# Performance work log

Hardware: AMD Instinct MI355X
Metric: run time of the kernel (lower is better)

## Reference

```python
import jax, jax.numpy as jnp
import numpy as np
import math

DIM = 1024
NUM_HEADS = 16
HEAD_DIM = DIM // NUM_HEADS
ROPE_BASE = 10000.0
LN_EPS = 1e-5


def _rope_tables(seq_len):
    inv_freq = 1.0 / (ROPE_BASE ** (jnp.arange(0, HEAD_DIM, 2, dtype=jnp.float32) / HEAD_DIM))
    t = jnp.arange(seq_len, dtype=jnp.float32)
    freqs = t[:, None] * inv_freq[None, :]            # (T, D/2)
    emb = jnp.concatenate([freqs, freqs], axis=-1)    # (T, D)
    return jnp.cos(emb), jnp.sin(emb)


def _rotate_half(x):
    x1 = x[..., ::2]
    x2 = x[..., 1::2]
    return jnp.stack((-x2, x1), axis=-1).reshape(x.shape)


def _heads(y):
    B, T, _ = y.shape
    return y.reshape(B, T, NUM_HEADS, HEAD_DIM).transpose(0, 2, 1, 3)  # (B,H,T,hd)


def _layernorm(x, w, b):
    mu = jnp.mean(x, axis=-1, keepdims=True)
    var = jnp.var(x, axis=-1, keepdims=True)
    return (x - mu) / jnp.sqrt(var + LN_EPS) * w + b


def setup_inputs() -> dict:
    key = jax.random.key(0)
    ks = jax.random.split(key, 16)
    s = 1.0 / math.sqrt(DIM)
    d = {
        "x": jax.random.normal(ks[0], (2, 2048, DIM), jnp.float32),
        "h_a": jax.random.normal(ks[1], (2, 512, DIM), jnp.float32),
        "h_t": jax.random.normal(ks[2], (2, 64, DIM), jnp.float32),
        "p": jax.random.normal(ks[3], (2, 256, DIM), jnp.float32),
    }
    names = ["Wq", "Wks", "Wvs", "Wka", "Wva", "Wkt", "Wvt", "Wo", "Wf"]
    for i, n in enumerate(names):
        d[n] = jax.random.normal(ks[4 + i], (DIM, DIM), jnp.float32) * s
        d["b" + n[1:]] = jnp.zeros((DIM,), jnp.float32)
    d["gating"] = jnp.zeros((1,), jnp.float32)
    d["ln_w"] = jnp.ones((DIM,), jnp.float32)
    d["ln_b"] = jnp.zeros((DIM,), jnp.float32)
    return d


def reference(x, h_a, h_t, p,
              Wq, bq, Wks, bks, Wvs, bvs, Wka, bka, Wva, bva,
              Wkt, bkt, Wvt, bvt, Wo, bo, Wf, bf,
              gating, ln_w, ln_b):
    B, T, D = x.shape
    g = jnp.tanh(gating)[0]
    h_adapter = jnp.concatenate((h_a, p), axis=1)          # (B, Ta+Tp, D)
    cos, sin = _rope_tables(T)                             # (T, hd)

    q = _heads(x @ Wq + bq)
    ks_ = _heads(x @ Wks + bks)
    vs = _heads(x @ Wvs + bvs)
    q = q * cos + _rotate_half(q) * sin
    ks_ = ks_ * cos + _rotate_half(ks_) * sin

    ka = _heads(h_adapter @ Wka + bka)
    va = _heads(h_adapter @ Wva + bva)
    kt = _heads(h_t @ Wkt + bkt)
    vt = _heads(h_t @ Wvt + bvt)

    s_self = jnp.einsum("bhqd,bhkd->bhqk", q, ks_)
    s_adpt = jnp.einsum("bhqd,bhkd->bhqk", q, ka)
    s_task = jnp.einsum("bhqd,bhkd->bhqk", q, kt) * g
    scores = jnp.concatenate([s_self, s_adpt, s_task], axis=-1) / math.sqrt(HEAD_DIM)
    attn = jax.nn.softmax(scores, axis=-1)                 # (B,H,T,S_total)

    v_all = jnp.concatenate([vs, va, vt], axis=2)          # (B,H,S_total,hd)
    out = jnp.einsum("bhqk,bhkd->bhqd", attn, v_all)
    out = out.transpose(0, 2, 1, 3).reshape(B, T, D)
    out = out @ Wo + bo

    res = _layernorm(out + x, ln_w, ln_b)
    res = jax.nn.relu(res @ Wf + bf)
    return res
```

## Files before the change

kernel.cpp:

```cpp
#include <hip/hip_runtime.h>

typedef __attribute__((ext_vector_type(8))) short bf16x8;
typedef __attribute__((ext_vector_type(4))) float f32x4;
typedef __attribute__((ext_vector_type(8))) unsigned short u16x8;
typedef __attribute__((ext_vector_type(4))) unsigned short u16x4;

#define DEV static __device__ __forceinline__

DEV float bf2f(unsigned short u) {
    union { unsigned int i; float f; } x; x.i = ((unsigned int)u) << 16; return x.f;
}
DEV unsigned short f2bf(float f) {
    union { float f; unsigned int i; } x; x.f = f;
    unsigned int r = x.i + 0x7FFFu + ((x.i >> 16) & 1u);
    return (unsigned short)(r >> 16);
}
DEV unsigned int cvt_pk_bf16(float a, float b) {
    unsigned int r;
    asm("v_cvt_pk_bf16_f32 %0, %1, %2" : "=v"(r) : "v"(a), "v"(b));
    return r;
}
DEV float ldany(const void* p, size_t i, bool f32) {
    return f32 ? ((const float*)p)[i] : bf2f(((const unsigned short*)p)[i]);
}
DEV void gload16(const void* g, void* l) {
    __builtin_amdgcn_global_load_lds(
        (const __attribute__((address_space(1))) unsigned int*)g,
        reinterpret_cast<__attribute__((address_space(3))) unsigned int*>(
            reinterpret_cast<uintptr_t>(l)),
        16, 0, 0);
}

struct Quad { const void* w0; const void* w1; const void* w2; const void* w3; };
struct Tri  { const void* b0; const void* b1; const void* b2; void* o0; void* o1; void* o2; };
struct ExtArgs {
    const void* ha; const void* pp; const void* ht;
    const void* bka; const void* bva; const void* bkt; const void* bvt;
    void* kx; void* vx;
};

__global__ __launch_bounds__(256)
void rope_tab(float2* __restrict__ tab, const unsigned int* __restrict__ wchk,
              int* __restrict__ flag)
{
    const int idx = blockIdx.x * 256 + threadIdx.x;
    if (idx == 0) flag[0] = (wchk[0] == 0x3F800000u) ? 1 : 0;
    const int m = idx >> 5, d = idx & 31;
    const float a = (float)m * exp2f(-(float)d * 0.41524101186092033f);
    float sn, cs;
    sincosf(a, &sn, &cs);
    tab[idx] = make_float2(cs, sn);
}

__global__ __launch_bounds__(256)
void transpose_w(Quad q, unsigned short* __restrict__ dstbase, const int* __restrict__ flagp)
{
    const bool dsf = (*flagp != 0);
    const int z = blockIdx.z;
    const void* W = (z == 0) ? q.w0 : (z == 1) ? q.w1 : (z == 2) ? q.w2 : q.w3;
    unsigned short* out = dstbase + ((size_t)z << 20);
    __shared__ unsigned short Ts[64][72];
    const int t = threadIdx.x;
    const int n0 = blockIdx.x * 64, k0 = blockIdx.y * 64;
    const int r = t >> 2, c = (t & 3) << 4;
    if (!dsf) {
        const unsigned short* Wp = (const unsigned short*)W + (size_t)(k0 + r) * 1024 + n0 + c;
        *(u16x8*)&Ts[r][c]     = *(const u16x8*)Wp;
        *(u16x8*)&Ts[r][c + 8] = *(const u16x8*)(Wp + 8);
    } else {
        const float4* Wf4 = (const float4*)((const float*)W + (size_t)(k0 + r) * 1024 + n0 + c);
        float4 f[4];
        #pragma unroll
        for (int j = 0; j < 4; ++j) f[j] = Wf4[j];
        unsigned int* Td = (unsigned int*)&Ts[r][c];
        #pragma unroll
        for (int j = 0; j < 4; ++j) {
            Td[2 * j]     = cvt_pk_bf16(f[j].x, f[j].y);
            Td[2 * j + 1] = cvt_pk_bf16(f[j].z, f[j].w);
        }
    }
    __syncthreads();
    unsigned short tmp[16];
    #pragma unroll
    for (int j = 0; j < 16; ++j) tmp[j] = Ts[c + j][r];
    unsigned short* op = out + (size_t)(n0 + r) * 1024 + k0 + c;
    *(u16x8*)op       = *(const u16x8*)&tmp[0];
    *(u16x8*)(op + 8) = *(const u16x8*)&tmp[8];
}

template<int AMODE, int OMODE, bool RELU, bool ROPEF>
__global__ __launch_bounds__(256)
void gemm_mfma(const void* __restrict__ A, const unsigned short* __restrict__ WTbase,
               Tri t3, const int* __restrict__ flagp, const float2* __restrict__ rtab,
               int mblocks, int rpb_in, int rpb_out, int row_off)
{
    const int K = 1024, N = 1024;
    const bool dsf = (*flagp != 0);
    const bool af32 = (AMODE == 1) && dsf;
    __shared__ unsigned short As[2][64 * 64];
    __shared__ unsigned short Bs[2][128 * 64];
    const int tid = threadIdx.x;
    const int z = blockIdx.y / mblocks;
    const int m0 = (blockIdx.y - z * mblocks) * 64;
    const int n0 = blockIdx.x * 128;
    const unsigned short* WT = WTbase + ((size_t)z << 20);
    const void* bias = (z == 0) ? t3.b0 : (z == 1) ? t3.b1 : t3.b2;
    void* Cv = (z == 0) ? t3.o0 : (z == 1) ? t3.o1 : t3.o2;

    const int lane = tid & 63, wv = tid >> 6;
    const int l3 = lane >> 3, c8 = lane & 7;
    const int swz = (c8 ^ l3) << 3;

    const unsigned short* Bsrc[4];
    #pragma unroll
    for (int j = 0; j < 4; ++j)
        Bsrc[j] = WT + (size_t)(n0 + (wv << 5) + (j << 3) + l3) * K + swz;
    const unsigned short* Asrc[2];
    #pragma unroll
    for (int j = 0; j < 2; ++j)
        Asrc[j] = (const unsigned short*)A + (size_t)(m0 + (wv << 4) + (j << 3) + l3) * K + swz;

    const int ar = tid >> 2, aq = (tid & 3) << 1, ah = ar & 7;
    const size_t arow = (size_t)(m0 + ar) * K + (aq << 3);

    const int wm = (wv >> 1) << 5, wn = (wv & 1) << 6;
    const int il = lane & 15, quad = lane >> 4;
    const int h = il & 7;
    const int c0 = ((quad ^ h) << 3);
    int aoff[2], boff[4];
    #pragma unroll
    for (int mi = 0; mi < 2; ++mi) aoff[mi] = (wm + mi * 16 + il) * 64;
    #pragma unroll
    for (int nj = 0; nj < 4; ++nj) boff[nj] = (wn + nj * 16 + il) * 64;

    f32x4 acc[2][4];
    #pragma unroll
    for (int mi = 0; mi < 2; ++mi)
        #pragma unroll
        for (int nj = 0; nj < 4; ++nj) acc[mi][nj] = (f32x4){0.f, 0.f, 0.f, 0.f};

    u16x8 av[2];
    auto loadA = [&](int kq) {
        if (!af32) {
            const unsigned short* Ag = (const unsigned short*)A + arow + kq;
            av[0] = *(const u16x8*)Ag;
            av[1] = *(const u16x8*)(Ag + 8);
        } else {
            const float4* Af4 = (const float4*)((const float*)A + arow + kq);
            float4 f[4];
            #pragma unroll
            for (int j = 0; j < 4; ++j) f[j] = Af4[j];
            #pragma unroll
            for (int j = 0; j < 2; ++j) {
                unsigned int* d = (unsigned int*)&av[j];
                d[0] = cvt_pk_bf16(f[2 * j].x, f[2 * j].y);
                d[1] = cvt_pk_bf16(f[2 * j].z, f[2 * j].w);
                d[2] = cvt_pk_bf16(f[2 * j + 1].x, f[2 * j + 1].y);
                d[3] = cvt_pk_bf16(f[2 * j + 1].z, f[2 * j + 1].w);
            }
        }
    };
    auto writeA = [&](int buf) {
        *(u16x8*)&As[buf][ar * 64 + ((aq ^ ah) << 3)]       = av[0];
        *(u16x8*)&As[buf][ar * 64 + (((aq ^ 1) ^ ah) << 3)] = av[1];
    };
    auto stageB = [&](int buf, int k0) {
        #pragma unroll
        for (int j = 0; j < 4; ++j)
            gload16(Bsrc[j] + k0, &Bs[buf][((wv << 2) + j) << 9]);
    };
    auto stageA = [&](int buf, int k0) {
        #pragma unroll
        for (int j = 0; j < 2; ++j)
            gload16(Asrc[j] + k0, &As[buf][((wv << 1) + j) << 9]);
    };

    if (AMODE == 1) loadA(0);
    stageB(0, 0);
    if (AMODE == 1) { writeA(0); loadA(64); }
    else            stageA(0, 0);
    __syncthreads();

    for (int k0 = 0; k0 < K; k0 += 64) {
        const int cur = (k0 >> 6) & 1;
        if (k0 + 64 < K) {
            stageB(cur ^ 1, k0 + 64);
            if (AMODE == 1) { writeA(cur ^ 1); if (k0 + 128 < K) loadA(k0 + 128); }
            else            stageA(cur ^ 1, k0 + 64);
        }
        #pragma unroll
        for (int kk = 0; kk < 2; ++kk) {
            const int cc = c0 ^ (kk << 5);
            bf16x8 af[2], bfr[4];
            #pragma unroll
            for (int mi = 0; mi < 2; ++mi) af[mi] = *(const bf16x8*)&As[cur][aoff[mi] + cc];
            #pragma unroll
            for (int nj = 0; nj < 4; ++nj) bfr[nj] = *(const bf16x8*)&Bs[cur][boff[nj] + cc];
            #pragma unroll
            for (int mi = 0; mi < 2; ++mi)
                #pragma unroll
                for (int nj = 0; nj < 4; ++nj)
                    acc[mi][nj] = __builtin_amdgcn_mfma_f32_16x16x32_bf16(
                        af[mi], bfr[nj], acc[mi][nj], 0, 0, 0);
        }
        __syncthreads();
    }

    const bool doRope = ROPEF && (z < 2);
    float bval[4];
    #pragma unroll
    for (int nj = 0; nj < 4; ++nj) bval[nj] = ldany(bias, n0 + wn + nj * 16 + il, dsf);
    #pragma unroll
    for (int mi = 0; mi < 2; ++mi) {
        #pragma unroll
        for (int r = 0; r < 4; ++r) {
            const int m = m0 + wm + mi * 16 + quad * 4 + r;
            const int bidx = m / rpb_in;
            const size_t orow = (size_t)bidx * rpb_out + row_off + (m - bidx * rpb_in);
            #pragma unroll
            for (int nj = 0; nj < 4; ++nj) {
                float v = acc[mi][nj][r] + bval[nj];
                if (doRope) {
                    const int dcol = n0 + wn + nj * 16 + il;
                    const float2 cs2 = rtab[((m & 2047) << 5) | (dcol & 31)];
                    const float partner = __shfl_xor(v, 1);
                    v = (il & 1) ? fmaf(v, cs2.x, partner * cs2.y)
                                 : fmaf(v, cs2.x, -partner * cs2.y);
                }
                if (RELU) v = fmaxf(v, 0.0f);
                const size_t idx = orow * N + n0 + wn + nj * 16 + il;
                if (OMODE == 0) ((unsigned short*)Cv)[idx] = f2bf(v);
                else {
                    if (dsf) ((float*)Cv)[idx] = v;
                    else     ((unsigned short*)Cv)[idx] = f2bf(v);
                }
            }
        }
    }
}

__global__ __launch_bounds__(256)
void gemm_ext(ExtArgs ea, const unsigned short* __restrict__ WTbase,
              const int* __restrict__ flagp)
{
    const int K = 1024, N = 1024;
    const bool dsf = (*flagp != 0);
    __shared__ unsigned short As[2][64 * 64];
    __shared__ unsigned short Bs[2][128 * 64];
    const int tid = threadIdx.x;
    const int y = blockIdx.y;
    const int w = (y >= 26) ? 1 : 0;
    const int yy = y - w * 26;
    int s, m0b;
    if (yy < 16)      { s = 0; m0b = yy; }
    else if (yy < 24) { s = 1; m0b = yy - 16; }
    else              { s = 2; m0b = yy - 24; }
    const void* A = (s == 0) ? ea.ha : (s == 1) ? ea.pp : ea.ht;
    const int rpb_in  = (s == 0) ? 512 : (s == 1) ? 256 : 64;
    const int row_off = (s == 0) ? 0 : (s == 1) ? 512 : 768;
    const int wtslot = ((s == 2) ? 2 : 0) + w;
    const void* bias = (w == 0) ? ((s == 2) ? ea.bkt : ea.bka)
                                : ((s == 2) ? ea.bvt : ea.bva);
    void* Cv = (w == 0) ? ea.kx : ea.vx;
    const int m0 = m0b * 64;
    const int n0 = blockIdx.x * 128;
    const unsigned short* WT = WTbase + ((size_t)wtslot << 20);

    const int lane = tid & 63, wv = tid >> 6;
    const int l3 = lane >> 3, c8 = lane & 7;
    const int swz = (c8 ^ l3) << 3;

    const unsigned short* Bsrc[4];
    #pragma unroll
    for (int j = 0; j < 4; ++j)
        Bsrc[j] = WT + (size_t)(n0 + (wv << 5) + (j << 3) + l3) * K + swz;

    const int ar = tid >> 2, aq = (tid & 3) << 1, ah = ar & 7;
    const size_t arow = (size_t)(m0 + ar) * K + (aq << 3);

    const int wm = (wv >> 1) << 5, wn = (wv & 1) << 6;
    const int il = lane & 15, quad = lane >> 4;
    const int h = il & 7;
    const int c0 = ((quad ^ h) << 3);
    int aoff[2], boff[4];
    #pragma unroll
    for (int mi = 0; mi < 2; ++mi) aoff[mi] = (wm + mi * 16 + il) * 64;
    #pragma unroll
    for (int nj = 0; nj < 4; ++nj) boff[nj] = (wn + nj * 16 + il) * 64;

    f32x4 acc[2][4];
    #pragma unroll
    for (int mi = 0; mi < 2; ++mi)
        #pragma unroll
        for (int nj = 0; nj < 4; ++nj) acc[mi][nj] = (f32x4){0.f, 0.f, 0.f, 0.f};

    u16x8 av[2];
    auto loadA = [&](int kq) {
        if (!dsf) {
            const unsigned short* Ag = (const unsigned short*)A + arow + kq;
            av[0] = *(const u16x8*)Ag;
            av[1] = *(const u16x8*)(Ag + 8);
        } else {
            const float4* Af4 = (const float4*)((const float*)A + arow + kq);
            float4 f[4];
            #pragma unroll
            for (int j = 0; j < 4; ++j) f[j] = Af4[j];
            #pragma unroll
            for (int j = 0; j < 2; ++j) {
                unsigned int* d = (unsigned int*)&av[j];
                d[0] = cvt_pk_bf16(f[2 * j].x, f[2 * j].y);
                d[1] = cvt_pk_bf16(f[2 * j].z, f[2 * j].w);
                d[2] = cvt_pk_bf16(f[2 * j + 1].x, f[2 * j + 1].y);
                d[3] = cvt_pk_bf16(f[2 * j + 1].z, f[2 * j + 1].w);
            }
        }
    };
    auto writeA = [&](int buf) {
        *(u16x8*)&As[buf][ar * 64 + ((aq ^ ah) << 3)]       = av[0];
        *(u16x8*)&As[buf][ar * 64 + (((aq ^ 1) ^ ah) << 3)] = av[1];
    };
    auto stageB = [&](int buf, int k0) {
        #pragma unroll
        for (int j = 0; j < 4; ++j)
            gload16(Bsrc[j] + k0, &Bs[buf][((wv << 2) + j) << 9]);
    };

    loadA(0);
    stageB(0, 0);
    writeA(0); loadA(64);
    __syncthreads();

    for (int k0 = 0; k0 < K; k0 += 64) {
        const int cur = (k0 >> 6) & 1;
        if (k0 + 64 < K) {
            stageB(cur ^ 1, k0 + 64);
            writeA(cur ^ 1);
            if (k0 + 128 < K) loadA(k0 + 128);
        }
        #pragma unroll
        for (int kk = 0; kk < 2; ++kk) {
            const int cc = c0 ^ (kk << 5);
            bf16x8 af[2], bfr[4];
            #pragma unroll
            for (int mi = 0; mi < 2; ++mi) af[mi] = *(const bf16x8*)&As[cur][aoff[mi] + cc];
            #pragma unroll
            for (int nj = 0; nj < 4; ++nj) bfr[nj] = *(const bf16x8*)&Bs[cur][boff[nj] + cc];
            #pragma unroll
            for (int mi = 0; mi < 2; ++mi)
                #pragma unroll
                for (int nj = 0; nj < 4; ++nj)
                    acc[mi][nj] = __builtin_amdgcn_mfma_f32_16x16x32_bf16(
                        af[mi], bfr[nj], acc[mi][nj], 0, 0, 0);
        }
        __syncthreads();
    }

    float bval[4];
    #pragma unroll
    for (int nj = 0; nj < 4; ++nj) bval[nj] = ldany(bias, n0 + wn + nj * 16 + il, dsf);
    #pragma unroll
    for (int mi = 0; mi < 2; ++mi) {
        #pragma unroll
        for (int r = 0; r < 4; ++r) {
            const int m = m0 + wm + mi * 16 + quad * 4 + r;
            const int bidx = m / rpb_in;
            const size_t orow = (size_t)bidx * 832 + row_off + (m - bidx * rpb_in);
            #pragma unroll
            for (int nj = 0; nj < 4; ++nj) {
                const float v = acc[mi][nj][r] + bval[nj];
                ((unsigned short*)Cv)[orow * N + n0 + wn + nj * 16 + il] = f2bf(v);
            }
        }
    }
}

__global__ __launch_bounds__(256)
void attn_mfma(const unsigned short* __restrict__ Q, const unsigned short* __restrict__ Ksf,
               const unsigned short* __restrict__ Vsf, const unsigned short* __restrict__ Kx,
               const unsigned short* __restrict__ Vx, const void* __restrict__ gate,
               const int* __restrict__ flagp, unsigned short* __restrict__ AO)
{
    const int T = 2048, TX = 832, D = 1024;
    __shared__ unsigned short Klds[2][64 * 72];
    __shared__ unsigned short Vlds[2][64 * 72];
    __shared__ unsigned short Plds[4][32 * 72];
    const int tid = threadIdx.x;
    const int bh = blockIdx.x;
    const int b = bh >> 4, h = bh & 15;
    const int t0 = blockIdx.y << 7;
    const bool dsf = (*flagp != 0);
    const float g = tanhf(ldany(gate, 0, dsf));

    const int lane = tid & 63, wv = tid >> 6;
    const int il = lane & 15, quad = lane >> 4;
    const int qw = t0 + (wv << 5);

    bf16x8 qf[2][2];
    #pragma unroll
    for (int mi = 0; mi < 2; ++mi) {
        const unsigned short* qp =
            Q + (size_t)(b * T + qw + mi * 16 + il) * D + (h << 6) + quad * 8;
        qf[mi][0] = *(const bf16x8*)qp;
        qf[mi][1] = *(const bf16x8*)(qp + 32);
    }
    bf16x8 ones;
    #pragma unroll
    for (int e = 0; e < 8; ++e) ((unsigned short*)&ones)[e] = 0x3F80;

    const int ksr = tid >> 2, ksd = (tid & 3) << 4;
    const int vkey = tid & 63, vdb = (tid >> 6) << 4;
    const int vpos = (vkey & 15) * 4 + (vkey >> 4);

    f32x4 o[2][4], ol[2];
    #pragma unroll
    for (int mi = 0; mi < 2; ++mi) {
        ol[mi] = (f32x4){0.f, 0.f, 0.f, 0.f};
        #pragma unroll
        for (int dt = 0; dt < 4; ++dt) o[mi][dt] = (f32x4){0.f, 0.f, 0.f, 0.f};
    }

    u16x8 kr0, kr1, vr0, vr1;
    auto load_kv = [&](int kt) {
        const unsigned short *kp, *vp;
        if (kt < 32) {
            kp = Ksf + (size_t)(b * T + (kt << 6) + ksr) * D + (h << 6) + ksd;
            vp = Vsf + (size_t)(b * T + (kt << 6) + vkey) * D + (h << 6) + vdb;
        } else {
            kp = Kx + (size_t)(b * TX + ((kt - 32) << 6) + ksr) * D + (h << 6) + ksd;
            vp = Vx + (size_t)(b * TX + ((kt - 32) << 6) + vkey) * D + (h << 6) + vdb;
        }
        kr0 = *(const u16x8*)kp; kr1 = *(const u16x8*)(kp + 8);
        vr0 = *(const u16x8*)vp; vr1 = *(const u16x8*)(vp + 8);
    };
    load_kv(0);

    #pragma unroll 1
    for (int kt = 0; kt < 45; ++kt) {
        const int cur = kt & 1;
        *(u16x8*)&Klds[cur][ksr * 72 + ksd]     = kr0;
        *(u16x8*)&Klds[cur][ksr * 72 + ksd + 8] = kr1;
        #pragma unroll
        for (int j = 0; j < 8; ++j)
            Vlds[cur][(vdb + j) * 72 + vpos]     = ((unsigned short*)&vr0)[j];
        #pragma unroll
        for (int j = 0; j < 8; ++j)
            Vlds[cur][(vdb + 8 + j) * 72 + vpos] = ((unsigned short*)&vr1)[j];
        __syncthreads();
        if (kt < 44) load_kv(kt + 1);

        f32x4 s[2][4];
        #pragma unroll
        for (int mi = 0; mi < 2; ++mi)
            #pragma unroll
            for (int ct = 0; ct < 4; ++ct) s[mi][ct] = (f32x4){0.f, 0.f, 0.f, 0.f};
        #pragma unroll
        for (int ct = 0; ct < 4; ++ct) {
            #pragma unroll
            for (int c = 0; c < 2; ++c) {
                bf16x8 kf = *(const bf16x8*)&Klds[cur][(ct * 16 + il) * 72 + c * 32 + quad * 8];
                #pragma unroll
                for (int mi = 0; mi < 2; ++mi)
                    s[mi][ct] = __builtin_amdgcn_mfma_f32_16x16x32_bf16(
                        qf[mi][c], kf, s[mi][ct], 0, 0, 0);
            }
        }
        const float fc = ((kt == 44) ? g : 1.0f) * 0.18033688011112042f;

        #pragma unroll
        for (int mi = 0; mi < 2; ++mi)
            #pragma unroll
            for (int r = 0; r < 4; ++r) {
                const float e0 = exp2f(fmaf(s[mi][0][r], fc, -11.541560327111708f));
                const float e1 = exp2f(fmaf(s[mi][1][r], fc, -11.541560327111708f));
                const float e2 = exp2f(fmaf(s[mi][2][r], fc, -11.541560327111708f));
                const float e3 = exp2f(fmaf(s[mi][3][r], fc, -11.541560327111708f));
                const unsigned int lo = cvt_pk_bf16(e0, e1);
                const unsigned int hi = cvt_pk_bf16(e2, e3);
                *(uint2*)&Plds[wv][(mi * 16 + quad * 4 + r) * 72 + (il << 2)] =
                    make_uint2(lo, hi);
            }

        #pragma unroll
        for (int c = 0; c < 2; ++c) {
            bf16x8 pf[2];
            #pragma unroll
            for (int mi = 0; mi < 2; ++mi)
                pf[mi] = *(const bf16x8*)&Plds[wv][(mi * 16 + il) * 72 + c * 32 + quad * 8];
            #pragma unroll
            for (int mi = 0; mi < 2; ++mi)
                ol[mi] = __builtin_amdgcn_mfma_f32_16x16x32_bf16(pf[mi], ones, ol[mi], 0, 0, 0);
            #pragma unroll
            for (int dt = 0; dt < 4; ++dt) {
                bf16x8 vf = *(const bf16x8*)&Vlds[cur][(dt * 16 + il) * 72 + c * 32 + quad * 8];
                #pragma unroll
                for (int mi = 0; mi < 2; ++mi)
                    o[mi][dt] = __builtin_amdgcn_mfma_f32_16x16x32_bf16(
                        pf[mi], vf, o[mi][dt], 0, 0, 0);
            }
        }
    }

    #pragma unroll
    for (int mi = 0; mi < 2; ++mi) {
        float invl[4];
        #pragma unroll
        for (int r = 0; r < 4; ++r) invl[r] = 1.0f / ol[mi][r];
        #pragma unroll
        for (int dt = 0; dt < 4; ++dt)
            #pragma unroll
            for (int r = 0; r < 4; ++r)
                AO[(size_t)(b * T + qw + mi * 16 + quad * 4 + r) * D + (h << 6) + dt * 16 + il] =
                    f2bf(o[mi][dt][r] * invl[r]);
    }
}

__global__ __launch_bounds__(256)
void ln_res(const unsigned short* __restrict__ proj, const void* __restrict__ x,
            const void* __restrict__ w, const void* __restrict__ bb,
            const int* __restrict__ flagp, unsigned short* __restrict__ y)
{
    const int row = blockIdx.x;
    const int tid = threadIdx.x;
    const bool dsf = (*flagp != 0);
    const unsigned short* pr = proj + (size_t)row * 1024;
    const u16x4 p4 = *(const u16x4*)(pr + (tid << 2));
    float v[4];
    if (dsf) {
        const float4 x4 = *(const float4*)((const float*)x + (size_t)row * 1024 + (tid << 2));
        v[0] = bf2f(p4[0]) + x4.x; v[1] = bf2f(p4[1]) + x4.y;
        v[2] = bf2f(p4[2]) + x4.z; v[3] = bf2f(p4[3]) + x4.w;
    } else {
        const u16x4 x4 = *(const u16x4*)((const unsigned short*)x + (size_t)row * 1024 + (tid << 2));
        #pragma unroll
        for (int e = 0; e < 4; ++e) v[e] = bf2f(p4[e]) + bf2f(x4[e]);
    }
    float s1 = v[0] + v[1] + v[2] + v[3];
    float s2 = v[0]*v[0] + v[1]*v[1] + v[2]*v[2] + v[3]*v[3];
    #pragma unroll
    for (int off = 1; off < 64; off <<= 1) {
        s1 += __shfl_xor(s1, off);
        s2 += __shfl_xor(s2, off);
    }
    __shared__ float red1[4], red2[4];
    const int wv = tid >> 6;
    if ((tid & 63) == 0) { red1[wv] = s1; red2[wv] = s2; }
    __syncthreads();
    s1 = red1[0] + red1[1] + red1[2] + red1[3];
    s2 = red2[0] + red2[1] + red2[2] + red2[3];
    const float mu = s1 * (1.0f / 1024.0f);
    const float var = s2 * (1.0f / 1024.0f) - mu * mu;
    const float rstd = rsqrtf(var + 1e-5f);
    float wv4[4], bv4[4];
    if (dsf) {
        const float4 wf = *(const float4*)((const float*)w + (tid << 2));
        const float4 bf4 = *(const float4*)((const float*)bb + (tid << 2));
        wv4[0] = wf.x; wv4[1] = wf.y; wv4[2] = wf.z; wv4[3] = wf.w;
        bv4[0] = bf4.x; bv4[1] = bf4.y; bv4[2] = bf4.z; bv4[3] = bf4.w;
    } else {
        const u16x4 wf = *(const u16x4*)((const unsigned short*)w + (tid << 2));
        const u16x4 bf4 = *(const u16x4*)((const unsigned short*)bb + (tid << 2));
        #pragma unroll
        for (int e = 0; e < 4; ++e) { wv4[e] = bf2f(wf[e]); bv4[e] = bf2f(bf4[e]); }
    }
    u16x4 o4;
    #pragma unroll
    for (int e = 0; e < 4; ++e)
        o4[e] = f2bf((v[e] - mu) * rstd * wv4[e] + bv4[e]);
    *(u16x4*)(y + (size_t)row * 1024 + (tid << 2)) = o4;
}

extern "C" void kernel_launch(void* const* d_in, const int* in_sizes, int n_in,
                              void* d_out, int out_size, void* d_ws, size_t ws_size,
                              hipStream_t stream)
{
    const void* x    = d_in[0];
    const void* h_a  = d_in[1];
    const void* h_t  = d_in[2];
    const void* p    = d_in[3];
    const void* Wq   = d_in[4];
    const void* bq   = d_in[5];
    const void* Wks  = d_in[6];
    const void* bks  = d_in[7];
    const void* Wvs  = d_in[8];
    const void* bvs  = d_in[9];
    const void* Wka  = d_in[10];
    const void* bka  = d_in[11];
    const void* Wva  = d_in[12];
    const void* bva  = d_in[13];
    const void* Wkt  = d_in[14];
    const void* bkt  = d_in[15];
    const void* Wvt  = d_in[16];
    const void* bvt  = d_in[17];
    const void* Wo   = d_in[18];
    const void* bo   = d_in[19];
    const void* Wf   = d_in[20];
    const void* bf_  = d_in[21];
    const void* gating = d_in[22];
    const void* ln_w = d_in[23];
    const void* ln_b = d_in[24];

    char* ws = (char*)d_ws;
    int*            flag = (int*)ws;
    unsigned short* qb   = (unsigned short*)(ws + 256);
    unsigned short* ks   = (unsigned short*)(ws + 8388864);
    unsigned short* vs   = (unsigned short*)(ws + 16777472);
    unsigned short* kx   = (unsigned short*)(ws + 25166080);
    unsigned short* vx   = (unsigned short*)(ws + 28573952);
    unsigned short* ao   = (unsigned short*)(ws + 31981824);
    unsigned short* proj  = ks;
    unsigned short* lnout = vs;
    unsigned short* WT1 = ao;
    unsigned short* WT3 = kx;
    float2*         rtab = (float2*)kx;

    dim3 blk(256);
    const Tri nul = {};

    rope_tab<<<256, blk, 0, stream>>>(rtab, (const unsigned int*)ln_w, flag);

    transpose_w<<<dim3(16, 16, 3), blk, 0, stream>>>(Quad{Wq, Wks, Wvs, Wvs}, WT1, flag);
    {
        Tri t3 = {bq, bks, bvs, qb, ks, vs};
        gemm_mfma<1, 0, false, true><<<dim3(8, 64 * 3), blk, 0, stream>>>(
            x, WT1, t3, flag, rtab, 64, 4096, 4096, 0);
    }

    transpose_w<<<dim3(16, 16, 4), blk, 0, stream>>>(Quad{Wka, Wva, Wkt, Wvt}, WT1, flag);
    {
        ExtArgs ea = {h_a, p, h_t, bka, bva, bkt, bvt, kx, vx};
        gemm_ext<<<dim3(8, 52), blk, 0, stream>>>(ea, WT1, flag);
    }

    attn_mfma<<<dim3(32, 16), blk, 0, stream>>>(qb, ks, vs, kx, vx, gating, flag, ao);

    transpose_w<<<dim3(16, 16, 2), blk, 0, stream>>>(Quad{Wo, Wf, Wf, Wf}, WT3, flag);
    {
        Tri t3 = {bo, nul.b1, nul.b2, proj, nul.o1, nul.o2};
        gemm_mfma<0, 0, false, false><<<dim3(8, 64), blk, 0, stream>>>(
            ao, WT3, t3, flag, nullptr, 64, 4096, 4096, 0);
    }
    ln_res<<<4096, blk, 0, stream>>>(proj, x, ln_w, ln_b, flag, lnout);
    {
        Tri t3 = {bf_, nul.b1, nul.b2, d_out, nul.o1, nul.o2};
        gemm_mfma<0, 2, true, false><<<dim3(8, 64), blk, 0, stream>>>(
            lnout, WT3 + ((size_t)1 << 20), t3, flag, nullptr, 64, 4096, 4096, 0);
    }
}
```

Baseline: 373.3 us.

## Merge projection GEMMs and weight transposes, vectorize V transpose in attention

Merges the seven front-end weight transposes into one launch and the QKV and adapter/task K/V projection GEMMs into a single gemm_front launch. Four of the transposed weights are staged in the output buffer so both sets can exist at once. In attention, the per-element scalar V transpose into LDS is replaced by strided 8-byte loads plus byte-permute packing, with an XOR swizzle on the V read side. exp2f is swapped for the hardware exp2 builtin. The aim is fewer launches, a fuller GPU for the small adapter GEMM, and less LDS store overhead, at the cost of heavier workspace aliasing.

After: 342.2 us. 1.09x faster.

```diff
diff --git a/kernel.cpp b/kernel.cpp
--- a/kernel.cpp
+++ b/kernel.cpp
@@ -33,10 +33,17 @@
 
 struct Quad { const void* w0; const void* w1; const void* w2; const void* w3; };
 struct Tri  { const void* b0; const void* b1; const void* b2; void* o0; void* o1; void* o2; };
-struct ExtArgs {
-    const void* ha; const void* pp; const void* ht;
+struct W7 {
+    const void* w0; const void* w1; const void* w2; const void* w3;
+    const void* w4; const void* w5; const void* w6;
+};
+struct FrontArgs {
+    const void* x; const void* ha; const void* pp; const void* ht;
+    const void* bq; const void* bks; const void* bvs;
     const void* bka; const void* bva; const void* bkt; const void* bvt;
-    void* kx; void* vx;
+    void* qb; void* ks; void* vs; void* kx; void* vx;
+    const unsigned short* wtp;
+    const unsigned short* wte;
 };
 
 __global__ __launch_bounds__(256)
@@ -53,12 +60,15 @@
 }
 
 __global__ __launch_bounds__(256)
-void transpose_w(Quad q, unsigned short* __restrict__ dstbase, const int* __restrict__ flagp)
+void transpose_w7(W7 q, unsigned short* __restrict__ dst1, unsigned short* __restrict__ dst2,
+                  int nsplit, const int* __restrict__ flagp)
 {
     const bool dsf = (*flagp != 0);
     const int z = blockIdx.z;
-    const void* W = (z == 0) ? q.w0 : (z == 1) ? q.w1 : (z == 2) ? q.w2 : q.w3;
-    unsigned short* out = dstbase + ((size_t)z << 20);
+    const void* W = (z == 0) ? q.w0 : (z == 1) ? q.w1 : (z == 2) ? q.w2 :
+                    (z == 3) ? q.w3 : (z == 4) ? q.w4 : (z == 5) ? q.w5 : q.w6;
+    unsigned short* out = (z < nsplit) ? dst1 + ((size_t)z << 20)
+                                       : dst2 + ((size_t)(z - nsplit) << 20);
     __shared__ unsigned short Ts[64][72];
     const int t = threadIdx.x;
     const int n0 = blockIdx.x * 64, k0 = blockIdx.y * 64;
@@ -88,15 +98,166 @@
     *(u16x8*)(op + 8) = *(const u16x8*)&tmp[8];
 }
 
-template<int AMODE, int OMODE, bool RELU, bool ROPEF>
 __global__ __launch_bounds__(256)
-void gemm_mfma(const void* __restrict__ A, const unsigned short* __restrict__ WTbase,
-               Tri t3, const int* __restrict__ flagp, const float2* __restrict__ rtab,
-               int mblocks, int rpb_in, int rpb_out, int row_off)
+void gemm_front(FrontArgs fa, const int* __restrict__ flagp, const float2* __restrict__ rtab)
 {
     const int K = 1024, N = 1024;
     const bool dsf = (*flagp != 0);
-    const bool af32 = (AMODE == 1) && dsf;
+    __shared__ unsigned short As[2][64 * 64];
+    __shared__ unsigned short Bs[2][128 * 64];
+    const int tid = threadIdx.x;
+    const int y = blockIdx.y;
+    const int n0 = blockIdx.x * 128;
+
+    const void* A; const unsigned short* WT; const void* bias; void* Cv;
+    int m0, rpb_in, rpb_o, row_off; bool rope;
+    if (y < 192) {
+        const int z = y >> 6;
+        m0 = (y & 63) << 6;
+        A = fa.x; WT = fa.wtp + ((size_t)z << 20);
+        bias = (z == 0) ? fa.bq : (z == 1) ? fa.bks : fa.bvs;
+        Cv   = (z == 0) ? fa.qb : (z == 1) ? fa.ks  : fa.vs;
+        rpb_in = 1 << 30; rpb_o = 0; row_off = 0;
+        rope = (z < 2);
+    } else {
+        const int yy0 = y - 192;
+        const int w = (yy0 >= 26) ? 1 : 0;
+        const int yy = yy0 - w * 26;
+        int s, m0b;
+        if (yy < 16)      { s = 0; m0b = yy; }
+        else if (yy < 24) { s = 1; m0b = yy - 16; }
+        else              { s = 2; m0b = yy - 24; }
+        A = (s == 0) ? fa.ha : (s == 1) ? fa.pp : fa.ht;
+        rpb_in  = (s == 0) ? 512 : (s == 1) ? 256 : 64;
+        row_off = (s == 0) ? 0 : (s == 1) ? 512 : 768;
+        WT   = fa.wte + ((size_t)(((s == 2) ? 2 : 0) + w) << 20);
+        bias = (w == 0) ? ((s == 2) ? fa.bkt : fa.bka) : ((s == 2) ? fa.bvt : fa.bva);
+        Cv   = (w == 0) ? fa.kx : fa.vx;
+        m0 = m0b << 6; rpb_o = 832; rope = false;
+    }
+
+    const int lane = tid & 63, wv = tid >> 6;
+    const int l3 = lane >> 3, c8 = lane & 7;
+    const int swz = (c8 ^ l3) << 3;
+
+    const unsigned short* Bsrc[4];
+    #pragma unroll
+    for (int j = 0; j < 4; ++j)
+        Bsrc[j] = WT + (size_t)(n0 + (wv << 5) + (j << 3) + l3) * K + swz;
+
+    const int ar = tid >> 2, aq = (tid & 3) << 1, ah = ar & 7;
+    const size_t arow = (size_t)(m0 + ar) * K + (aq << 3);
+
+    const int wm = (wv >> 1) << 5, wn = (wv & 1) << 6;
+    const int il = lane & 15, quad = lane >> 4;
+    const int h = il & 7;
+    const int c0 = ((quad ^ h) << 3);
+    int aoff[2], boff[4];
+    #pragma unroll
+    for (int mi = 0; mi < 2; ++mi) aoff[mi] = (wm + mi * 16 + il) * 64;
+    #pragma unroll
+    for (int nj = 0; nj < 4; ++nj) boff[nj] = (wn + nj * 16 + il) * 64;
+
+    f32x4 acc[2][4];
+    #pragma unroll
+    for (int mi = 0; mi < 2; ++mi)
+        #pragma unroll
+        for (int nj = 0; nj < 4; ++nj) acc[mi][nj] = (f32x4){0.f, 0.f, 0.f, 0.f};
+
+    u16x8 av[2];
+    auto loadA = [&](int kq) {
+        if (!dsf) {
+            const unsigned short* Ag = (const unsigned short*)A + arow + kq;
+            av[0] = *(const u16x8*)Ag;
+            av[1] = *(const u16x8*)(Ag + 8);
+        } else {
+            const float4* Af4 = (const float4*)((const float*)A + arow + kq);
+            float4 f[4];
+            #pragma unroll
+            for (int j = 0; j < 4; ++j) f[j] = Af4[j];
+            #pragma unroll
+            for (int j = 0; j < 2; ++j) {
+                unsigned int* d = (unsigned int*)&av[j];
+                d[0] = cvt_pk_bf16(f[2 * j].x, f[2 * j].y);
+                d[1] = cvt_pk_bf16(f[2 * j].z, f[2 * j].w);
+                d[2] = cvt_pk_bf16(f[2 * j + 1].x, f[2 * j + 1].y);
+                d[3] = cvt_pk_bf16(f[2 * j + 1].z, f[2 * j + 1].w);
+            }
+        }
+    };
+    auto writeA = [&](int buf) {
+        *(u16x8*)&As[buf][ar * 64 + ((aq ^ ah) << 3)]       = av[0];
+        *(u16x8*)&As[buf][ar * 64 + (((aq ^ 1) ^ ah) << 3)] = av[1];
+    };
+    auto stageB = [&](int buf, int k0) {
+        #pragma unroll
+        for (int j = 0; j < 4; ++j)
+            gload16(Bsrc[j] + k0, &Bs[buf][((wv << 2) + j) << 9]);
+    };
+
+    loadA(0);
+    stageB(0, 0);
+    writeA(0); loadA(64);
+    __syncthreads();
+
+    for (int k0 = 0; k0 < K; k0 += 64) {
+        const int cur = (k0 >> 6) & 1;
+        if (k0 + 64 < K) {
+            stageB(cur ^ 1, k0 + 64);
+            writeA(cur ^ 1);
+            if (k0 + 128 < K) loadA(k0 + 128);
+        }
+        #pragma unroll
+        for (int kk = 0; kk < 2; ++kk) {
+            const int cc = c0 ^ (kk << 5);
+            bf16x8 af[2], bfr[4];
+            #pragma unroll
+            for (int mi = 0; mi < 2; ++mi) af[mi] = *(const bf16x8*)&As[cur][aoff[mi] + cc];
+            #pragma unroll
+            for (int nj = 0; nj < 4; ++nj) bfr[nj] = *(const bf16x8*)&Bs[cur][boff[nj] + cc];
+            #pragma unroll
+            for (int mi = 0; mi < 2; ++mi)
+                #pragma unroll
+                for (int nj = 0; nj < 4; ++nj)
+                    acc[mi][nj] = __builtin_amdgcn_mfma_f32_16x16x32_bf16(
+                        af[mi], bfr[nj], acc[mi][nj], 0, 0, 0);
+        }
+        __syncthreads();
+    }
+
+    float bval[4];
+    #pragma unroll
+    for (int nj = 0; nj < 4; ++nj) bval[nj] = ldany(bias, n0 + wn + nj * 16 + il, dsf);
+    #pragma unroll
+    for (int mi = 0; mi < 2; ++mi) {
+        #pragma unroll
+        for (int r = 0; r < 4; ++r) {
+            const int m = m0 + wm + mi * 16 + quad * 4 + r;
+            const int bidx = m / rpb_in;
+            const size_t orow = (size_t)bidx * rpb_o + row_off + (m - bidx * rpb_in);
+            #pragma unroll
+            for (int nj = 0; nj < 4; ++nj) {
+                float v = acc[mi][nj][r] + bval[nj];
+                if (rope) {
+                    const int dcol = n0 + wn + nj * 16 + il;
+                    const float2 cs2 = rtab[((m & 2047) << 5) | (dcol & 31)];
+                    const float partner = __shfl_xor(v, 1);
+                    v = (il & 1) ? fmaf(v, cs2.x, partner * cs2.y)
+                                 : fmaf(v, cs2.x, -partner * cs2.y);
+                }
+                ((unsigned short*)Cv)[orow * N + n0 + wn + nj * 16 + il] = f2bf(v);
+            }
+        }
+    }
+}
+
+template<int OMODE, bool RELU>
+__global__ __launch_bounds__(256)
+void gemm_mfma(const void* __restrict__ A, const unsigned short* __restrict__ WTbase,
+               Tri t3, const int* __restrict__ flagp, int mblocks)
+{
+    const int K = 1024, N = 1024;
+    const bool dsf = (*flagp != 0);
     __shared__ unsigned short As[2][64 * 64];
     __shared__ unsigned short Bs[2][128 * 64];
     const int tid = threadIdx.x;
@@ -120,9 +281,6 @@
     for (int j = 0; j < 2; ++j)
         Asrc[j] = (const unsigned short*)A + (size_t)(m0 + (wv << 4) + (j << 3) + l3) * K + swz;
 
-    const int ar = tid >> 2, aq = (tid & 3) << 1, ah = ar & 7;
-    const size_t arow = (size_t)(m0 + ar) * K + (aq << 3);
-
     const int wm = (wv >> 1) << 5, wn = (wv & 1) << 6;
     const int il = lane & 15, quad = lane >> 4;
     const int h = il & 7;
@@ -139,31 +297,6 @@
         #pragma unroll
         for (int nj = 0; nj < 4; ++nj) acc[mi][nj] = (f32x4){0.f, 0.f, 0.f, 0.f};
 
-    u16x8 av[2];
-    auto loadA = [&](int kq) {
-        if (!af32) {
-            const unsigned short* Ag = (const unsigned short*)A + arow + kq;
-            av[0] = *(const u16x8*)Ag;
-            av[1] = *(const u16x8*)(Ag + 8);
-        } else {
-            const float4* Af4 = (const float4*)((const float*)A + arow + kq);
-            float4 f[4];
-            #pragma unroll
-            for (int j = 0; j < 4; ++j) f[j] = Af4[j];
-            #pragma unroll
-            for (int j = 0; j < 2; ++j) {
-                unsigned int* d = (unsigned int*)&av[j];
-                d[0] = cvt_pk_bf16(f[2 * j].x, f[2 * j].y);
-                d[1] = cvt_pk_bf16(f[2 * j].z, f[2 * j].w);
-                d[2] = cvt_pk_bf16(f[2 * j + 1].x, f[2 * j + 1].y);
-                d[3] = cvt_pk_bf16(f[2 * j + 1].z, f[2 * j + 1].w);
-            }
-        }
-    };
-    auto writeA = [&](int buf) {
-        *(u16x8*)&As[buf][ar * 64 + ((aq ^ ah) << 3)]       = av[0];
-        *(u16x8*)&As[buf][ar * 64 + (((aq ^ 1) ^ ah) << 3)] = av[1];
-    };
     auto stageB = [&](int buf, int k0) {
         #pragma unroll
         for (int j = 0; j < 4; ++j)
@@ -175,18 +308,15 @@
             gload16(Asrc[j] + k0, &As[buf][((wv << 1) + j) << 9]);
     };
 
-    if (AMODE == 1) loadA(0);
     stageB(0, 0);
-    if (AMODE == 1) { writeA(0); loadA(64); }
-    else            stageA(0, 0);
+    stageA(0, 0);
     __syncthreads();
 
     for (int k0 = 0; k0 < K; k0 += 64) {
         const int cur = (k0 >> 6) & 1;
         if (k0 + 64 < K) {
             stageB(cur ^ 1, k0 + 64);
-            if (AMODE == 1) { writeA(cur ^ 1); if (k0 + 128 < K) loadA(k0 + 128); }
-            else            stageA(cur ^ 1, k0 + 64);
+            stageA(cur ^ 1, k0 + 64);
         }
         #pragma unroll
         for (int kk = 0; kk < 2; ++kk) {
@@ -206,7 +336,6 @@
         __syncthreads();
     }
 
-    const bool doRope = ROPEF && (z < 2);
     float bval[4];
     #pragma unroll
     for (int nj = 0; nj < 4; ++nj) bval[nj] = ldany(bias, n0 + wn + nj * 16 + il, dsf);
@@ -214,19 +343,10 @@
     for (int mi = 0; mi < 2; ++mi) {
         #pragma unroll
         for (int r = 0; r < 4; ++r) {
-            const int m = m0 + wm + mi * 16 + quad * 4 + r;
-            const int bidx = m / rpb_in;
-            const size_t orow = (size_t)bidx * rpb_out + row_off + (m - bidx * rpb_in);
+            const size_t orow = (size_t)(m0 + wm + mi * 16 + quad * 4 + r);
             #pragma unroll
             for (int nj = 0; nj < 4; ++nj) {
                 float v = acc[mi][nj][r] + bval[nj];
-                if (doRope) {
-                    const int dcol = n0 + wn + nj * 16 + il;
-                    const float2 cs2 = rtab[((m & 2047) << 5) | (dcol & 31)];
-                    const float partner = __shfl_xor(v, 1);
-                    v = (il & 1) ? fmaf(v, cs2.x, partner * cs2.y)
-                                 : fmaf(v, cs2.x, -partner * cs2.y);
-                }
                 if (RELU) v = fmaxf(v, 0.0f);
                 const size_t idx = orow * N + n0 + wn + nj * 16 + il;
                 if (OMODE == 0) ((unsigned short*)Cv)[idx] = f2bf(v);
@@ -234,141 +354,6 @@
                     if (dsf) ((float*)Cv)[idx] = v;
                     else     ((unsigned short*)Cv)[idx] = f2bf(v);
                 }
-            }
-        }
-    }
-}
-
-__global__ __launch_bounds__(256)
-void gemm_ext(ExtArgs ea, const unsigned short* __restrict__ WTbase,
-              const int* __restrict__ flagp)
-{
-    const int K = 1024, N = 1024;
-    const bool dsf = (*flagp != 0);
-    __shared__ unsigned short As[2][64 * 64];
-    __shared__ unsigned short Bs[2][128 * 64];
-    const int tid = threadIdx.x;
-    const int y = blockIdx.y;
-    const int w = (y >= 26) ? 1 : 0;
-    const int yy = y - w * 26;
-    int s, m0b;
-    if (yy < 16)      { s = 0; m0b = yy; }
-    else if (yy < 24) { s = 1; m0b = yy - 16; }
-    else              { s = 2; m0b = yy - 24; }
-    const void* A = (s == 0) ? ea.ha : (s == 1) ? ea.pp : ea.ht;
-    const int rpb_in  = (s == 0) ? 512 : (s == 1) ? 256 : 64;
-    const int row_off = (s == 0) ? 0 : (s == 1) ? 512 : 768;
-    const int wtslot = ((s == 2) ? 2 : 0) + w;
-    const void* bias = (w == 0) ? ((s == 2) ? ea.bkt : ea.bka)
-                                : ((s == 2) ? ea.bvt : ea.bva);
-    void* Cv = (w == 0) ? ea.kx : ea.vx;
-    const int m0 = m0b * 64;
-    const int n0 = blockIdx.x * 128;
-    const unsigned short* WT = WTbase + ((size_t)wtslot << 20);
-
-    const int lane = tid & 63, wv = tid >> 6;
-    const int l3 = lane >> 3, c8 = lane & 7;
-    const int swz = (c8 ^ l3) << 3;
-
-    const unsigned short* Bsrc[4];
-    #pragma unroll
-    for (int j = 0; j < 4; ++j)
-        Bsrc[j] = WT + (size_t)(n0 + (wv << 5) + (j << 3) + l3) * K + swz;
-
-    const int ar = tid >> 2, aq = (tid & 3) << 1, ah = ar & 7;
-    const size_t arow = (size_t)(m0 + ar) * K + (aq << 3);
-
-    const int wm = (wv >> 1) << 5, wn = (wv & 1) << 6;
-    const int il = lane & 15, quad = lane >> 4;
-    const int h = il & 7;
-    const int c0 = ((quad ^ h) << 3);
-    int aoff[2], boff[4];
-    #pragma unroll
-    for (int mi = 0; mi < 2; ++mi) aoff[mi] = (wm + mi * 16 + il) * 64;
-    #pragma unroll
-    for (int nj = 0; nj < 4; ++nj) boff[nj] = (wn + nj * 16 + il) * 64;
-
-    f32x4 acc[2][4];
-    #pragma unroll
-    for (int mi = 0; mi < 2; ++mi)
-        #pragma unroll
-        for (int nj = 0; nj < 4; ++nj) acc[mi][nj] = (f32x4){0.f, 0.f, 0.f, 0.f};
-
-    u16x8 av[2];
-    auto loadA = [&](int kq) {
-        if (!dsf) {
-            const unsigned short* Ag = (const unsigned short*)A + arow + kq;
-            av[0] = *(const u16x8*)Ag;
-            av[1] = *(const u16x8*)(Ag + 8);
-        } else {
-            const float4* Af4 = (const float4*)((const float*)A + arow + kq);
-            float4 f[4];
-            #pragma unroll
-            for (int j = 0; j < 4; ++j) f[j] = Af4[j];
-            #pragma unroll
-            for (int j = 0; j < 2; ++j) {
-                unsigned int* d = (unsigned int*)&av[j];
-                d[0] = cvt_pk_bf16(f[2 * j].x, f[2 * j].y);
-                d[1] = cvt_pk_bf16(f[2 * j].z, f[2 * j].w);
-                d[2] = cvt_pk_bf16(f[2 * j + 1].x, f[2 * j + 1].y);
-                d[3] = cvt_pk_bf16(f[2 * j + 1].z, f[2 * j + 1].w);
-            }
-        }
-    };
-    auto writeA = [&](int buf) {
-        *(u16x8*)&As[buf][ar * 64 + ((aq ^ ah) << 3)]       = av[0];
-        *(u16x8*)&As[buf][ar * 64 + (((aq ^ 1) ^ ah) << 3)] = av[1];
-    };
-    auto stageB = [&](int buf, int k0) {
-        #pragma unroll
-        for (int j = 0; j < 4; ++j)
-            gload16(Bsrc[j] + k0, &Bs[buf][((wv << 2) + j) << 9]);
-    };
-
-    loadA(0);
-    stageB(0, 0);
-    writeA(0); loadA(64);
-    __syncthreads();
-
-    for (int k0 = 0; k0 < K; k0 += 64) {
-        const int cur = (k0 >> 6) & 1;
-        if (k0 + 64 < K) {
-            stageB(cur ^ 1, k0 + 64);
-            writeA(cur ^ 1);
-            if (k0 + 128 < K) loadA(k0 + 128);
-        }
-        #pragma unroll
-        for (int kk = 0; kk < 2; ++kk) {
-            const int cc = c0 ^ (kk << 5);
-            bf16x8 af[2], bfr[4];
-            #pragma unroll
-            for (int mi = 0; mi < 2; ++mi) af[mi] = *(const bf16x8*)&As[cur][aoff[mi] + cc];
-            #pragma unroll
-            for (int nj = 0; nj < 4; ++nj) bfr[nj] = *(const bf16x8*)&Bs[cur][boff[nj] + cc];
-            #pragma unroll
-            for (int mi = 0; mi < 2; ++mi)
-                #pragma unroll
-                for (int nj = 0; nj < 4; ++nj)
-                    acc[mi][nj] = __builtin_amdgcn_mfma_f32_16x16x32_bf16(
-                        af[mi], bfr[nj], acc[mi][nj], 0, 0, 0);
-        }
-        __syncthreads();
-    }
-
-    float bval[4];
-    #pragma unroll
-    for (int nj = 0; nj < 4; ++nj) bval[nj] = ldany(bias, n0 + wn + nj * 16 + il, dsf);
-    #pragma unroll
-    for (int mi = 0; mi < 2; ++mi) {
-        #pragma unroll
-        for (int r = 0; r < 4; ++r) {
-            const int m = m0 + wm + mi * 16 + quad * 4 + r;
-            const int bidx = m / rpb_in;
-            const size_t orow = (size_t)bidx * 832 + row_off + (m - bidx * rpb_in);
-            #pragma unroll
-            for (int nj = 0; nj < 4; ++nj) {
-                const float v = acc[mi][nj][r] + bval[nj];
-                ((unsigned short*)Cv)[orow * N + n0 + wn + nj * 16 + il] = f2bf(v);
             }
         }
     }
@@ -408,8 +393,9 @@
     for (int e = 0; e < 8; ++e) ((unsigned short*)&ones)[e] = 0x3F80;
 
     const int ksr = tid >> 2, ksd = (tid & 3) << 4;
-    const int vkey = tid & 63, vdb = (tid >> 6) << 4;
-    const int vpos = (vkey & 15) * 4 + (vkey >> 4);
+    const int t16 = tid >> 4, dg = tid & 15;
+    const int vwcol = ((((t16 >> 1) ^ (dg & 3)) << 3) | ((t16 & 1) << 2));
+    const int vwrow = (dg << 2) * 72 + vwcol;
 
     f32x4 o[2][4], ol[2];
     #pragma unroll
@@ -419,34 +405,49 @@
         for (int dt = 0; dt < 4; ++dt) o[mi][dt] = (f32x4){0.f, 0.f, 0.f, 0.f};
     }
 
-    u16x8 kr0, kr1, vr0, vr1;
-    auto load_kv = [&](int kt) {
-        const unsigned short *kp, *vp;
-        if (kt < 32) {
-            kp = Ksf + (size_t)(b * T + (kt << 6) + ksr) * D + (h << 6) + ksd;
-            vp = Vsf + (size_t)(b * T + (kt << 6) + vkey) * D + (h << 6) + vdb;
-        } else {
-            kp = Kx + (size_t)(b * TX + ((kt - 32) << 6) + ksr) * D + (h << 6) + ksd;
-            vp = Vx + (size_t)(b * TX + ((kt - 32) << 6) + vkey) * D + (h << 6) + vdb;
-        }
+    const unsigned short* kp = Ksf + (size_t)(b * T + ksr) * D + (h << 6) + ksd;
+    const unsigned short* vp = Vsf + (size_t)(b * T + t16) * D + (h << 6) + (dg << 2);
+
+    u16x8 kr0, kr1;
+    uint2 vm0, vm1, vm2, vm3;
+    auto load_kv = [&]() {
         kr0 = *(const u16x8*)kp; kr1 = *(const u16x8*)(kp + 8);
-        vr0 = *(const u16x8*)vp; vr1 = *(const u16x8*)(vp + 8);
+        vm0 = *(const uint2*)vp;
+        vm1 = *(const uint2*)(vp + (1 << 14));
+        vm2 = *(const uint2*)(vp + (2 << 14));
+        vm3 = *(const uint2*)(vp + (3 << 14));
     };
-    load_kv(0);
+    load_kv();
 
     #pragma unroll 1
     for (int kt = 0; kt < 45; ++kt) {
         const int cur = kt & 1;
         *(u16x8*)&Klds[cur][ksr * 72 + ksd]     = kr0;
         *(u16x8*)&Klds[cur][ksr * 72 + ksd + 8] = kr1;
-        #pragma unroll
-        for (int j = 0; j < 8; ++j)
-            Vlds[cur][(vdb + j) * 72 + vpos]     = ((unsigned short*)&vr0)[j];
-        #pragma unroll
-        for (int j = 0; j < 8; ++j)
-            Vlds[cur][(vdb + 8 + j) * 72 + vpos] = ((unsigned short*)&vr1)[j];
+        {
+            unsigned int p00 = __builtin_amdgcn_perm(vm1.x, vm0.x, 0x05040100);
+            unsigned int p01 = __builtin_amdgcn_perm(vm3.x, vm2.x, 0x05040100);
+            unsigned int p10 = __builtin_amdgcn_perm(vm1.x, vm0.x, 0x07060302);
+            unsigned int p11 = __builtin_amdgcn_perm(vm3.x, vm2.x, 0x07060302);
+            unsigned int p20 = __builtin_amdgcn_perm(vm1.y, vm0.y, 0x05040100);
+            unsigned int p21 = __builtin_amdgcn_perm(vm3.y, vm2.y, 0x05040100);
+            unsigned int p30 = __builtin_amdgcn_perm(vm1.y, vm0.y, 0x07060302);
+            unsigned int p31 = __builtin_amdgcn_perm(vm3.y, vm2.y, 0x07060302);
+            *(uint2*)&Vlds[cur][vwrow]           = make_uint2(p00, p01);
+            *(uint2*)&Vlds[cur][vwrow + 72]      = make_uint2(p10, p11);
+            *(uint2*)&Vlds[cur][vwrow + 144]     = make_uint2(p20, p21);
+            *(uint2*)&Vlds[cur][vwrow + 216]     = make_uint2(p30, p31);
+        }
         __syncthreads();
-        if (kt < 44) load_kv(kt + 1);
+        if (kt < 44) {
+            if (kt == 31) {
+                kp = Kx + (size_t)(b * TX + ksr) * D + (h << 6) + ksd;
+                vp = Vx + (size_t)(b * TX + t16) * D + (h << 6) + (dg << 2);
+            } else {
+                kp += (size_t)64 * D; vp += (size_t)64 * D;
+            }
+            load_kv();
+        }
 
         f32x4 s[2][4];
         #pragma unroll
@@ -470,10 +471,10 @@
         for (int mi = 0; mi < 2; ++mi)
             #pragma unroll
             for (int r = 0; r < 4; ++r) {
-                const float e0 = exp2f(fmaf(s[mi][0][r], fc, -11.541560327111708f));
-                const float e1 = exp2f(fmaf(s[mi][1][r], fc, -11.541560327111708f));
-                const float e2 = exp2f(fmaf(s[mi][2][r], fc, -11.541560327111708f));
-                const float e3 = exp2f(fmaf(s[mi][3][r], fc, -11.541560327111708f));
+                const float e0 = __builtin_amdgcn_exp2f(fmaf(s[mi][0][r], fc, -11.541560327111708f));
+                const float e1 = __builtin_amdgcn_exp2f(fmaf(s[mi][1][r], fc, -11.541560327111708f));
+                const float e2 = __builtin_amdgcn_exp2f(fmaf(s[mi][2][r], fc, -11.541560327111708f));
+                const float e3 = __builtin_amdgcn_exp2f(fmaf(s[mi][3][r], fc, -11.541560327111708f));
                 const unsigned int lo = cvt_pk_bf16(e0, e1);
                 const unsigned int hi = cvt_pk_bf16(e2, e3);
                 *(uint2*)&Plds[wv][(mi * 16 + quad * 4 + r) * 72 + (il << 2)] =
@@ -491,7 +492,8 @@
                 ol[mi] = __builtin_amdgcn_mfma_f32_16x16x32_bf16(pf[mi], ones, ol[mi], 0, 0, 0);
             #pragma unroll
             for (int dt = 0; dt < 4; ++dt) {
-                bf16x8 vf = *(const bf16x8*)&Vlds[cur][(dt * 16 + il) * 72 + c * 32 + quad * 8];
+                bf16x8 vf = *(const bf16x8*)
+                    &Vlds[cur][(dt * 16 + il) * 72 + c * 32 + ((quad ^ (il >> 2)) << 3)];
                 #pragma unroll
                 for (int mi = 0; mi < 2; ++mi)
                     o[mi][dt] = __builtin_amdgcn_mfma_f32_16x16x32_bf16(
@@ -610,39 +612,41 @@
     unsigned short* proj  = ks;
     unsigned short* lnout = vs;
     unsigned short* WT1 = ao;
+    unsigned short* WTd = (unsigned short*)d_out;
     unsigned short* WT3 = kx;
-    float2*         rtab = (float2*)kx;
+    float2*         rtab = (float2*)(ws + 31981824 + 6291456);
 
     dim3 blk(256);
     const Tri nul = {};
 
     rope_tab<<<256, blk, 0, stream>>>(rtab, (const unsigned int*)ln_w, flag);
 
-    transpose_w<<<dim3(16, 16, 3), blk, 0, stream>>>(Quad{Wq, Wks, Wvs, Wvs}, WT1, flag);
     {
-        Tri t3 = {bq, bks, bvs, qb, ks, vs};
-        gemm_mfma<1, 0, false, true><<<dim3(8, 64 * 3), blk, 0, stream>>>(
-            x, WT1, t3, flag, rtab, 64, 4096, 4096, 0);
-    }
-
-    transpose_w<<<dim3(16, 16, 4), blk, 0, stream>>>(Quad{Wka, Wva, Wkt, Wvt}, WT1, flag);
+        W7 w7 = {Wq, Wks, Wvs, Wka, Wva, Wkt, Wvt};
+        transpose_w7<<<dim3(16, 16, 7), blk, 0, stream>>>(w7, WT1, WTd, 3, flag);
+    }
+
     {
-        ExtArgs ea = {h_a, p, h_t, bka, bva, bkt, bvt, kx, vx};
-        gemm_ext<<<dim3(8, 52), blk, 0, stream>>>(ea, WT1, flag);
+        FrontArgs fa = {x, h_a, p, h_t,
+                        bq, bks, bvs, bka, bva, bkt, bvt,
+                        qb, ks, vs, kx, vx, WT1, WTd};
+        gemm_front<<<dim3(8, 244), blk, 0, stream>>>(fa, flag, rtab);
     }
 
     attn_mfma<<<dim3(32, 16), blk, 0, stream>>>(qb, ks, vs, kx, vx, gating, flag, ao);
 
-    transpose_w<<<dim3(16, 16, 2), blk, 0, stream>>>(Quad{Wo, Wf, Wf, Wf}, WT3, flag);
+    {
+        W7 w2 = {Wo, Wf, Wf, Wf, Wf, Wf, Wf};
+        transpose_w7<<<dim3(16, 16, 2), blk, 0, stream>>>(w2, WT3, WT3, 2, flag);
+    }
     {
         Tri t3 = {bo, nul.b1, nul.b2, proj, nul.o1, nul.o2};
-        gemm_mfma<0, 0, false, false><<<dim3(8, 64), blk, 0, stream>>>(
-            ao, WT3, t3, flag, nullptr, 64, 4096, 4096, 0);
+        gemm_mfma<0, false><<<dim3(8, 64), blk, 0, stream>>>(ao, WT3, t3, flag, 64);
     }
     ln_res<<<4096, blk, 0, stream>>>(proj, x, ln_w, ln_b, flag, lnout);
     {
         Tri t3 = {bf_, nul.b1, nul.b2, d_out, nul.o1, nul.o2};
-        gemm_mfma<0, 2, true, false><<<dim3(8, 64), blk, 0, stream>>>(
-            lnout, WT3 + ((size_t)1 << 20), t3, flag, nullptr, 64, 4096, 4096, 0);
-    }
-}
+        gemm_mfma<2, true><<<dim3(8, 64), blk, 0, stream>>>(
+            lnout, WT3 + ((size_t)1 << 20), t3, flag, 64);
+    }
+}
```
